# Kernel tuning notes

Hardware: AMD Instinct MI355X
Metric: run time of the kernel (lower is better)

Reference implementation:

```python
import jax, jax.numpy as jnp
import numpy as np

B, T, D_MODEL, N_HEADS = 4, 2048, 1024, 16
D_K = D_MODEL // N_HEADS


def setup_inputs() -> dict:
    key = jax.random.key(0)
    kx, kq, kk, kv, ko = jax.random.split(key, 5)
    scale = 1.0 / np.sqrt(D_MODEL)  # ~ torch Linear init scale
    return {
        "x": jax.random.normal(kx, (B, T, D_MODEL), dtype=jnp.float32),
        "W_q": jax.random.uniform(kq, (D_MODEL, D_MODEL), jnp.float32, -scale, scale),
        "W_k": jax.random.uniform(kk, (D_MODEL, D_MODEL), jnp.float32, -scale, scale),
        "W_v": jax.random.uniform(kv, (D_MODEL, D_MODEL), jnp.float32, -scale, scale),
        "W_o": jax.random.uniform(ko, (D_MODEL, D_MODEL), jnp.float32, -scale, scale),
    }


def reference(x, W_q, W_k, W_v, W_o):
    b, t, _ = x.shape
    # nn.Linear(y) = y @ W.T ; split to (B, H, T, d_k)
    def split_heads(y):
        return y.reshape(b, t, N_HEADS, D_K).transpose(0, 2, 1, 3)

    Q = split_heads(x @ W_q.T)
    K = split_heads(x @ W_k.T)
    V = split_heads(x @ W_v.T)

    scores = jnp.einsum("bhqd,bhkd->bhqk", Q, K) / jnp.sqrt(jnp.float32(D_K))
    causal = jnp.triu(jnp.ones((t, t), dtype=bool), k=1)  # True = masked
    scores = jnp.where(causal, -jnp.inf, scores)
    weights = jax.nn.softmax(scores, axis=-1)
    out = jnp.einsum("bhqk,bhkd->bhqd", weights, V)
    out = out.transpose(0, 2, 1, 3).reshape(b, t, D_MODEL)
    return out @ W_o.T
```

## Files before the change

### kernel.cpp

```cpp
#include <hip/hip_runtime.h>

typedef __attribute__((ext_vector_type(8))) short s16x8;
typedef __attribute__((ext_vector_type(4))) float fx4;
typedef __attribute__((ext_vector_type(4))) int ix4;

#define B_SZ 4
#define T_SZ 2048
#define DM 1024
#define NH 16
#define DK 64
#define M_SZ (B_SZ * T_SZ)
#define NINF (-__builtin_inff())
#define QSCALE (0.125f * 1.44269504088896340736f)

__device__ __forceinline__ unsigned short f2bf(float f) {
    unsigned int u = __float_as_uint(f);
    unsigned int r = u + 0x7fffu + ((u >> 16) & 1u);
    return (unsigned short)(r >> 16);
}

__device__ __forceinline__ unsigned cvtpk(float lo, float hi) {
    unsigned r;
    asm("v_cvt_pk_bf16_f32 %0, %1, %2" : "=v"(r) : "v"(lo), "v"(hi));
    return r;
}

__device__ __forceinline__ void async16(const unsigned short* g, unsigned short* l) {
    __builtin_amdgcn_global_load_lds(
        (const __attribute__((address_space(1))) unsigned int*)g,
        (__attribute__((address_space(3))) unsigned int*)l, 16, 0, 0);
}

__device__ __forceinline__ void barrier_nodrain() {
    asm volatile("" ::: "memory");
    __builtin_amdgcn_s_barrier();
    asm volatile("" ::: "memory");
}

__global__ void cast_all(const float* __restrict__ x,
                         const float* __restrict__ s1, const float* __restrict__ s2,
                         const float* __restrict__ s3, const float* __restrict__ s4,
                         unsigned short* __restrict__ xb, unsigned short* __restrict__ wb) {
    const int y = blockIdx.y;
    const float* s;
    unsigned short* d;
    int n;
    if (y == 0) { s = x; d = xb; n = M_SZ * DM; }
    else {
        s = (y == 1) ? s1 : (y == 2) ? s2 : (y == 3) ? s3 : s4;
        d = wb + (size_t)(y - 1) * (DM * DM);
        n = DM * DM;
    }
    int i = (blockIdx.x * blockDim.x + threadIdx.x) * 4;
    int stride = gridDim.x * blockDim.x * 4;
    for (; i + 3 < n; i += stride) {
        float4 v = *(const float4*)(s + i);
        ushort4 o;
        o.x = f2bf(v.x); o.y = f2bf(v.y); o.z = f2bf(v.z); o.w = f2bf(v.w);
        *(ushort4*)(d + i) = o;
    }
}

__global__ __launch_bounds__(512, 2) void gemm_qkv256(const unsigned short* __restrict__ A,
                                                      const unsigned short* __restrict__ W,
                                                      unsigned short* __restrict__ Qs,
                                                      unsigned short* __restrict__ Kb,
                                                      unsigned short* __restrict__ Vt) {
    __shared__ __align__(16) unsigned short S[49152];

    const int t = threadIdx.x;
    const int lane = t & 63, w = t >> 6;
    const int wm = w >> 2, wn = w & 3;
    const int lrow = lane & 15, lk = lane >> 4;
    const int bx = blockIdx.x;
    const int m0 = blockIdx.y * 128;
    const int K = DM;
    const int NKT = K / 64;

    fx4 acc[4][4] = {};

    const int srow = t >> 3;
    const int cs = (t & 7) ^ (srow & 7);
    const unsigned short* Ag = A + (long)(m0 + srow) * K + cs * 8;
    const unsigned short* Bg = W + (long)(bx * 256 + srow) * K + cs * 8;

    async16(Ag,           &S[t * 8]);
    async16(Ag + 64 * K,  &S[4096 + t * 8]);
    async16(Bg,           &S[16384 + t * 8]);
    async16(Bg + 64 * K,  &S[16384 + 4096 + t * 8]);
    async16(Bg + 128 * K, &S[16384 + 8192 + t * 8]);
    async16(Bg + 192 * K, &S[16384 + 12288 + t * 8]);

    for (int kt = 0; kt < NKT; ++kt) {
        const int cur = kt & 1;
        if (kt + 1 < NKT) {
            const int ko = (kt + 1) * 64;
            const int nbA = (cur ^ 1) * 8192;
            const int nbB = 16384 + (cur ^ 1) * 16384;
            async16(Ag + ko,           &S[nbA + t * 8]);
            async16(Ag + 64 * K + ko,  &S[nbA + 4096 + t * 8]);
            async16(Bg + ko,           &S[nbB + t * 8]);
            async16(Bg + 64 * K + ko,  &S[nbB + 4096 + t * 8]);
            async16(Bg + 128 * K + ko, &S[nbB + 8192 + t * 8]);
            async16(Bg + 192 * K + ko, &S[nbB + 12288 + t * 8]);
            asm volatile("s_waitcnt vmcnt(6)" ::: "memory");
        } else {
            asm volatile("s_waitcnt vmcnt(0)" ::: "memory");
        }
        barrier_nodrain();
        const unsigned short* Ab = &S[cur * 8192];
        const unsigned short* Bb = &S[16384 + cur * 16384];
#pragma unroll
        for (int kk = 0; kk < 2; ++kk) {
            const int sw = ((kk * 4 + lk) ^ (lrow & 7)) * 8;
            s16x8 af[4], bf[4];
#pragma unroll
            for (int mf = 0; mf < 4; ++mf)
                af[mf] = *(const s16x8*)&Ab[(wm * 64 + mf * 16 + lrow) * 64 + sw];
#pragma unroll
            for (int nf = 0; nf < 4; ++nf)
                bf[nf] = *(const s16x8*)&Bb[(wn * 64 + nf * 16 + lrow) * 64 + sw];
            __builtin_amdgcn_s_setprio(1);
#pragma unroll
            for (int mf = 0; mf < 4; ++mf)
#pragma unroll
                for (int nf = 0; nf < 4; ++nf)
                    acc[mf][nf] = __builtin_amdgcn_mfma_f32_16x16x32_bf16(af[mf], bf[nf], acc[mf][nf], 0, 0, 0);
            __builtin_amdgcn_s_setprio(0);
        }
        barrier_nodrain();
    }

    const int which = bx >> 2;
    const int n0l = (bx & 3) * 256;
    if (which < 2) {
        unsigned short* dst = which ? Kb : Qs;
        const float sc = which ? 1.f : QSCALE;
#pragma unroll
        for (int mf = 0; mf < 4; ++mf)
#pragma unroll
            for (int nf = 0; nf < 4; ++nf)
#pragma unroll
                for (int r = 0; r < 4; ++r) {
                    int row = m0 + wm * 64 + mf * 16 + lk * 4 + r;
                    int col = n0l + wn * 64 + nf * 16 + lrow;
                    dst[(long)row * DM + col] = f2bf(acc[mf][nf][r] * sc);
                }
    } else {
#pragma unroll
        for (int mf = 0; mf < 4; ++mf)
#pragma unroll
            for (int nf = 0; nf < 4; ++nf) {
                const int cl = wn * 64 + nf * 16 + lrow;
                const int rl = wm * 64 + mf * 16 + lk * 4;
                ushort4 pk;
                pk.x = f2bf(acc[mf][nf][0]); pk.y = f2bf(acc[mf][nf][1]);
                pk.z = f2bf(acc[mf][nf][2]); pk.w = f2bf(acc[mf][nf][3]);
                *(ushort4*)&S[cl * 132 + rl] = pk;
            }
        __syncthreads();
        const int c = t >> 1, h2 = t & 1;
        unsigned short* vtp = Vt + (long)(n0l + c) * M_SZ + m0 + h2 * 64;
#pragma unroll
        for (int j = 0; j < 8; ++j) {
            union { struct { ushort4 a, b; } s; ix4 v; } u;
            u.s.a = *(const ushort4*)&S[c * 132 + h2 * 64 + j * 8];
            u.s.b = *(const ushort4*)&S[c * 132 + h2 * 64 + j * 8 + 4];
            *(ix4*)(vtp + j * 8) = u.v;
        }
    }
}

__global__ __launch_bounds__(512, 2) void gemm_out256(const unsigned short* __restrict__ A,
                                                      const unsigned short* __restrict__ W,
                                                      float* __restrict__ C) {
    __shared__ __align__(16) unsigned short S[49152];

    const int t = threadIdx.x;
    const int lane = t & 63, w = t >> 6;
    const int wm = w >> 2, wn = w & 3;
    const int lrow = lane & 15, lk = lane >> 4;
    const int n0 = blockIdx.x * 256;
    const int m0 = blockIdx.y * 128;
    const int K = DM;
    const int NKT = K / 64;

    fx4 acc[4][4] = {};

    const int srow = t >> 3;
    const int cs = (t & 7) ^ (srow & 7);
    const unsigned short* Ag = A + (long)(m0 + srow) * K + cs * 8;
    const unsigned short* Bg = W + (long)(n0 + srow) * K + cs * 8;

    async16(Ag,           &S[t * 8]);
    async16(Ag + 64 * K,  &S[4096 + t * 8]);
    async16(Bg,           &S[16384 + t * 8]);
    async16(Bg + 64 * K,  &S[16384 + 4096 + t * 8]);
    async16(Bg + 128 * K, &S[16384 + 8192 + t * 8]);
    async16(Bg + 192 * K, &S[16384 + 12288 + t * 8]);

    for (int kt = 0; kt < NKT; ++kt) {
        const int cur = kt & 1;
        if (kt + 1 < NKT) {
            const int ko = (kt + 1) * 64;
            const int nbA = (cur ^ 1) * 8192;
            const int nbB = 16384 + (cur ^ 1) * 16384;
            async16(Ag + ko,           &S[nbA + t * 8]);
            async16(Ag + 64 * K + ko,  &S[nbA + 4096 + t * 8]);
            async16(Bg + ko,           &S[nbB + t * 8]);
            async16(Bg + 64 * K + ko,  &S[nbB + 4096 + t * 8]);
            async16(Bg + 128 * K + ko, &S[nbB + 8192 + t * 8]);
            async16(Bg + 192 * K + ko, &S[nbB + 12288 + t * 8]);
            asm volatile("s_waitcnt vmcnt(6)" ::: "memory");
        } else {
            asm volatile("s_waitcnt vmcnt(0)" ::: "memory");
        }
        barrier_nodrain();
        const unsigned short* Ab = &S[cur * 8192];
        const unsigned short* Bb = &S[16384 + cur * 16384];
#pragma unroll
        for (int kk = 0; kk < 2; ++kk) {
            const int sw = ((kk * 4 + lk) ^ (lrow & 7)) * 8;
            s16x8 af[4], bf[4];
#pragma unroll
            for (int mf = 0; mf < 4; ++mf)
                af[mf] = *(const s16x8*)&Ab[(wm * 64 + mf * 16 + lrow) * 64 + sw];
#pragma unroll
            for (int nf = 0; nf < 4; ++nf)
                bf[nf] = *(const s16x8*)&Bb[(wn * 64 + nf * 16 + lrow) * 64 + sw];
            __builtin_amdgcn_s_setprio(1);
#pragma unroll
            for (int mf = 0; mf < 4; ++mf)
#pragma unroll
                for (int nf = 0; nf < 4; ++nf)
                    acc[mf][nf] = __builtin_amdgcn_mfma_f32_16x16x32_bf16(af[mf], bf[nf], acc[mf][nf], 0, 0, 0);
            __builtin_amdgcn_s_setprio(0);
        }
        barrier_nodrain();
    }

#pragma unroll
    for (int mf = 0; mf < 4; ++mf)
#pragma unroll
        for (int nf = 0; nf < 4; ++nf)
#pragma unroll
            for (int r = 0; r < 4; ++r) {
                int row = m0 + wm * 64 + mf * 16 + lk * 4 + r;
                int col = n0 + wn * 64 + nf * 16 + lrow;
                C[(long)row * DM + col] = acc[mf][nf][r];
            }
}

__global__ __launch_bounds__(256, 4) void attn_kernel(const unsigned short* __restrict__ Q,
                                                      const unsigned short* __restrict__ Kb,
                                                      const unsigned short* __restrict__ Vt,
                                                      unsigned short* __restrict__ O) {
    __shared__ __align__(16) unsigned short Ks[2][64 * 64];
    __shared__ __align__(16) unsigned short Vs[2][64 * 64];
    __shared__ __align__(16) unsigned short Pl[4][16 * 64];

    const int t = threadIdx.x;
    const int lane = t & 63, w = t >> 6;
    const int lrow = lane & 15, lk = lane >> 4;
    const int hb = blockIdx.x;
    const int h = hb & 15, b = hb >> 4;
    const int qb = 15 - blockIdx.y;
    const int row0 = b * T_SZ;
    const int q0w = qb * 128 + w * 32;

    s16x8 qf[2][2];
#pragma unroll
    for (int hh = 0; hh < 2; ++hh) {
        const unsigned short* qp = Q + (long)(row0 + q0w + hh * 16 + lrow) * DM + h * DK + lk * 8;
        qf[hh][0] = *(const s16x8*)qp;
        qf[hh][1] = *(const s16x8*)(qp + 32);
    }

    fx4 acc[2][4] = {};
    float mrun[2] = {NINF, NINF}, lsum[2] = {0.f, 0.f};

    const int srow = t >> 3;
    const int chk = (t & 7) ^ (srow & 7);
    const unsigned short* Kg = Kb + (long)(row0 + srow) * DM + h * DK + chk * 8;
    const unsigned short* Vg = Vt + (long)(h * DK + srow) * M_SZ + row0 + chk * 8;
    unsigned short* Kl = &Ks[0][t * 8];
    unsigned short* Vl = &Vs[0][t * 8];

    const int nt = 2 * qb + 2;

    async16(Kg, Kl);
    async16(Kg + 32 * DM, Kl + 2048);
    async16(Vg, Vl);
    async16(Vg + 32 * (long)M_SZ, Vl + 2048);
    asm volatile("s_waitcnt vmcnt(0)" ::: "memory");
    __syncthreads();

    for (int kt = 0; kt < nt; ++kt) {
        const int cur = kt & 1;
        const bool pre = (kt + 1 < nt);
        if (pre) {
            const long koff = (long)(kt + 1) * 64 * DM;
            const int voff = (kt + 1) * 64;
            async16(Kg + koff, Kl + (cur ^ 1) * 4096);
            async16(Kg + koff + 32 * DM, Kl + (cur ^ 1) * 4096 + 2048);
            async16(Vg + voff, Vl + (cur ^ 1) * 4096);
            async16(Vg + voff + 32 * (long)M_SZ, Vl + (cur ^ 1) * 4096 + 2048);
        }
        const int kv0 = kt * 64;
        if (kv0 <= q0w + 31) {
            const char* ksb = (const char*)&Ks[cur][0];
            float p[2][4][4];
#pragma unroll
            for (int sub = 0; sub < 4; ++sub) {
                const int kv0s = kv0 + sub * 16;
                if (kv0s <= q0w + 31) {
                    const int rb = (sub * 16 + lrow) << 7;
                    const int sw = (lrow & 7) << 4;
                    const s16x8 kf0 = *(const s16x8*)(ksb + (rb + ((lk * 16) ^ sw)));
                    const s16x8 kf1 = *(const s16x8*)(ksb + (rb + ((64 + lk * 16) ^ sw)));
                    fx4 s1 = {};
                    s1 = __builtin_amdgcn_mfma_f32_16x16x32_bf16(kf0, qf[1][0], s1, 0, 0, 0);
                    s1 = __builtin_amdgcn_mfma_f32_16x16x32_bf16(kf1, qf[1][1], s1, 0, 0, 0);
                    if (kv0s + 15 > q0w + 16) {
#pragma unroll
                        for (int r = 0; r < 4; ++r)
                            if (kv0s + lk * 4 + r > q0w + 16 + lrow) s1[r] = NINF;
                    }
#pragma unroll
                    for (int r = 0; r < 4; ++r) p[1][sub][r] = s1[r];
                    if (kv0s <= q0w + 15) {
                        fx4 s0 = {};
                        s0 = __builtin_amdgcn_mfma_f32_16x16x32_bf16(kf0, qf[0][0], s0, 0, 0, 0);
                        s0 = __builtin_amdgcn_mfma_f32_16x16x32_bf16(kf1, qf[0][1], s0, 0, 0, 0);
                        if (kv0s + 15 > q0w) {
#pragma unroll
                            for (int r = 0; r < 4; ++r)
                                if (kv0s + lk * 4 + r > q0w + lrow) s0[r] = NINF;
                        }
#pragma unroll
                        for (int r = 0; r < 4; ++r) p[0][sub][r] = s0[r];
                    } else {
#pragma unroll
                        for (int r = 0; r < 4; ++r) p[0][sub][r] = NINF;
                    }
                } else {
#pragma unroll
                    for (int r = 0; r < 4; ++r) { p[0][sub][r] = NINF; p[1][sub][r] = NINF; }
                }
            }
#pragma unroll
            for (int hh = 0; hh < 2; ++hh) {
                float m0 = fmaxf(fmaxf(p[hh][0][0], p[hh][0][1]), fmaxf(p[hh][0][2], p[hh][0][3]));
                float m1 = fmaxf(fmaxf(p[hh][1][0], p[hh][1][1]), fmaxf(p[hh][1][2], p[hh][1][3]));
                float m2 = fmaxf(fmaxf(p[hh][2][0], p[hh][2][1]), fmaxf(p[hh][2][2], p[hh][2][3]));
                float m3 = fmaxf(fmaxf(p[hh][3][0], p[hh][3][1]), fmaxf(p[hh][3][2], p[hh][3][3]));
                float pm = fmaxf(fmaxf(m0, m1), fmaxf(m2, m3));
                if (__any(pm > mrun[hh] + 8.f)) {
                    pm = fmaxf(pm, __shfl_xor(pm, 16));
                    pm = fmaxf(pm, __shfl_xor(pm, 32));
                    const float mnew = fmaxf(mrun[hh], pm);
                    const float sc = exp2f(mrun[hh] - mnew);
                    mrun[hh] = mnew;
                    lsum[hh] *= sc;
#pragma unroll
                    for (int r = 0; r < 4; ++r) {
                        const float scr = __shfl(sc, lk * 4 + r);
                        acc[hh][0][r] *= scr; acc[hh][1][r] *= scr;
                        acc[hh][2][r] *= scr; acc[hh][3][r] *= scr;
                    }
                }
#pragma unroll
                for (int sub = 0; sub < 4; ++sub)
#pragma unroll
                    for (int r = 0; r < 4; ++r)
                        p[hh][sub][r] = exp2f(p[hh][sub][r] - mrun[hh]);
                float a0 = (p[hh][0][0] + p[hh][0][1]) + (p[hh][0][2] + p[hh][0][3]);
                float a1 = (p[hh][1][0] + p[hh][1][1]) + (p[hh][1][2] + p[hh][1][3]);
                float a2 = (p[hh][2][0] + p[hh][2][1]) + (p[hh][2][2] + p[hh][2][3]);
                float a3 = (p[hh][3][0] + p[hh][3][1]) + (p[hh][3][2] + p[hh][3][3]);
                lsum[hh] += (a0 + a1) + (a2 + a3);
            }
            s16x8 pf[2][2];
#pragma unroll
            for (int hh = 0; hh < 2; ++hh) {
#pragma unroll
                for (int sub = 0; sub < 4; ++sub) {
                    uint2 pw;
                    pw.x = cvtpk(p[hh][sub][0], p[hh][sub][1]);
                    pw.y = cvtpk(p[hh][sub][2], p[hh][sub][3]);
                    *(uint2*)&Pl[w][lrow * 64 + ((sub * 16 + lk * 4) ^ ((lrow & 7) << 3))] = pw;
                }
                pf[hh][0] = *(const s16x8*)&Pl[w][lrow * 64 + ((lk * 8) ^ ((lrow & 7) << 3))];
                pf[hh][1] = *(const s16x8*)&Pl[w][lrow * 64 + ((32 + lk * 8) ^ ((lrow & 7) << 3))];
            }
#pragma unroll
            for (int s = 0; s < 2; ++s) {
                if (kv0 + s * 32 <= q0w + 31) {
                    const bool h0a = (kv0 + s * 32 <= q0w + 15);
#pragma unroll
                    for (int nf = 0; nf < 4; ++nf) {
                        const int d = nf * 16 + lrow;
                        const s16x8 vf = *(const s16x8*)&Vs[cur][d * 64 + (((s * 4 + lk) ^ (lrow & 7)) << 3)];
                        if (h0a)
                            acc[0][nf] = __builtin_amdgcn_mfma_f32_16x16x32_bf16(pf[0][s], vf, acc[0][nf], 0, 0, 0);
                        acc[1][nf] = __builtin_amdgcn_mfma_f32_16x16x32_bf16(pf[1][s], vf, acc[1][nf], 0, 0, 0);
                    }
                }
            }
        }
        asm volatile("s_waitcnt vmcnt(0)" ::: "memory");
        __syncthreads();
    }

#pragma unroll
    for (int hh = 0; hh < 2; ++hh) {
        lsum[hh] += __shfl_xor(lsum[hh], 16);
        lsum[hh] += __shfl_xor(lsum[hh], 32);
        float linv[4];
#pragma unroll
        for (int r = 0; r < 4; ++r) linv[r] = 1.f / __shfl(lsum[hh], lk * 4 + r);
        unsigned short* op = O + (long)(row0 + q0w + hh * 16) * DM + h * DK;
#pragma unroll
        for (int nf = 0; nf < 4; ++nf)
#pragma unroll
            for (int r = 0; r < 4; ++r)
                op[(long)(lk * 4 + r) * DM + nf * 16 + lrow] = f2bf(acc[hh][nf][r] * linv[r]);
    }
}

extern "C" void kernel_launch(void* const* d_in, const int* in_sizes, int n_in,
                              void* d_out, int out_size, void* d_ws, size_t ws_size,
                              hipStream_t stream) {
    const float* x  = (const float*)d_in[0];
    const float* Wq = (const float*)d_in[1];
    const float* Wk = (const float*)d_in[2];
    const float* Wv = (const float*)d_in[3];
    const float* Wo = (const float*)d_in[4];
    float* out = (float*)d_out;

    unsigned short* wsu = (unsigned short*)d_ws;
    unsigned short* xb  = wsu;
    unsigned short* wqb = xb + 8388608;
    unsigned short* wob = wqb + 3 * 1048576;
    unsigned short* Qs  = wob + 1048576;
    unsigned short* Ob  = Qs + 8388608;

    unsigned short* Kb = (unsigned short*)d_out;
    unsigned short* Vt = Kb + 8388608;

    cast_all<<<dim3(512, 5), 256, 0, stream>>>(x, Wq, Wk, Wv, Wo, xb, wqb);

    gemm_qkv256<<<dim3(12, M_SZ / 128), 512, 0, stream>>>(xb, wqb, Qs, Kb, Vt);

    dim3 agrid(64, 16);
    attn_kernel<<<agrid, 256, 0, stream>>>(Qs, Kb, Vt, Ob);

    gemm_out256<<<dim3(DM / 256, M_SZ / 128), 512, 0, stream>>>(Ob, wob, out);
}
```

Baseline: 178.6 us.

## Triple-buffer GEMM loads and compute softmax row sums with MFMA

Both projection GEMMs move from double to triple buffering in shared memory, prefetching two K-tiles ahead with adjusted vmcnt waits, to hide more global load latency. Shared memory per block grows from 96KB to 144KB, which may prevent two blocks fitting per CU. In attention, the softmax denominator is now accumulated by an MFMA of the bf16 probabilities against a ones vector, replacing per-lane float adds and the final cross-lane shuffles. The max reduction is also regrouped into three-input max operations. The MFMA row sum uses bf16-rounded probabilities, matching the values used in the PV product.

```diff
diff --git a/kernel.cpp b/kernel.cpp
--- a/kernel.cpp
+++ b/kernel.cpp
@@ -12,6 +12,7 @@
 #define M_SZ (B_SZ * T_SZ)
 #define NINF (-__builtin_inff())
 #define QSCALE (0.125f * 1.44269504088896340736f)
+#define MAX3(a,b,c) fmaxf(fmaxf(a,b),c)
 
 __device__ __forceinline__ unsigned short f2bf(float f) {
     unsigned int u = __float_as_uint(f);
@@ -66,7 +67,7 @@
                                                       unsigned short* __restrict__ Qs,
                                                       unsigned short* __restrict__ Kb,
                                                       unsigned short* __restrict__ Vt) {
-    __shared__ __align__(16) unsigned short S[49152];
+    __shared__ __align__(16) unsigned short S[73728];
 
     const int t = threadIdx.x;
     const int lane = t & 63, w = t >> 6;
@@ -84,32 +85,41 @@
     const unsigned short* Ag = A + (long)(m0 + srow) * K + cs * 8;
     const unsigned short* Bg = W + (long)(bx * 256 + srow) * K + cs * 8;
 
-    async16(Ag,           &S[t * 8]);
-    async16(Ag + 64 * K,  &S[4096 + t * 8]);
-    async16(Bg,           &S[16384 + t * 8]);
-    async16(Bg + 64 * K,  &S[16384 + 4096 + t * 8]);
-    async16(Bg + 128 * K, &S[16384 + 8192 + t * 8]);
-    async16(Bg + 192 * K, &S[16384 + 12288 + t * 8]);
-
+#pragma unroll
+    for (int pt = 0; pt < 2; ++pt) {
+        const int ko = pt * 64;
+        const int nbA = pt * 8192;
+        const int nbB = 24576 + pt * 16384;
+        async16(Ag + ko,           &S[nbA + t * 8]);
+        async16(Ag + 64 * K + ko,  &S[nbA + 4096 + t * 8]);
+        async16(Bg + ko,           &S[nbB + t * 8]);
+        async16(Bg + 64 * K + ko,  &S[nbB + 4096 + t * 8]);
+        async16(Bg + 128 * K + ko, &S[nbB + 8192 + t * 8]);
+        async16(Bg + 192 * K + ko, &S[nbB + 12288 + t * 8]);
+    }
+
+    int cur = 0;
     for (int kt = 0; kt < NKT; ++kt) {
-        const int cur = kt & 1;
-        if (kt + 1 < NKT) {
-            const int ko = (kt + 1) * 64;
-            const int nbA = (cur ^ 1) * 8192;
-            const int nbB = 16384 + (cur ^ 1) * 16384;
+        if (kt + 2 < NKT) {
+            int stg = cur + 2; if (stg >= 3) stg -= 3;
+            const int ko = (kt + 2) * 64;
+            const int nbA = stg * 8192;
+            const int nbB = 24576 + stg * 16384;
             async16(Ag + ko,           &S[nbA + t * 8]);
             async16(Ag + 64 * K + ko,  &S[nbA + 4096 + t * 8]);
             async16(Bg + ko,           &S[nbB + t * 8]);
             async16(Bg + 64 * K + ko,  &S[nbB + 4096 + t * 8]);
             async16(Bg + 128 * K + ko, &S[nbB + 8192 + t * 8]);
             async16(Bg + 192 * K + ko, &S[nbB + 12288 + t * 8]);
+            asm volatile("s_waitcnt vmcnt(12)" ::: "memory");
+        } else if (kt + 1 < NKT) {
             asm volatile("s_waitcnt vmcnt(6)" ::: "memory");
         } else {
             asm volatile("s_waitcnt vmcnt(0)" ::: "memory");
         }
         barrier_nodrain();
         const unsigned short* Ab = &S[cur * 8192];
-        const unsigned short* Bb = &S[16384 + cur * 16384];
+        const unsigned short* Bb = &S[24576 + cur * 16384];
 #pragma unroll
         for (int kk = 0; kk < 2; ++kk) {
             const int sw = ((kk * 4 + lk) ^ (lrow & 7)) * 8;
@@ -129,6 +139,7 @@
             __builtin_amdgcn_s_setprio(0);
         }
         barrier_nodrain();
+        cur = (cur + 1 == 3) ? 0 : cur + 1;
     }
 
     const int which = bx >> 2;
@@ -174,7 +185,7 @@
 __global__ __launch_bounds__(512, 2) void gemm_out256(const unsigned short* __restrict__ A,
                                                       const unsigned short* __restrict__ W,
                                                       float* __restrict__ C) {
-    __shared__ __align__(16) unsigned short S[49152];
+    __shared__ __align__(16) unsigned short S[73728];
 
     const int t = threadIdx.x;
     const int lane = t & 63, w = t >> 6;
@@ -192,32 +203,41 @@
     const unsigned short* Ag = A + (long)(m0 + srow) * K + cs * 8;
     const unsigned short* Bg = W + (long)(n0 + srow) * K + cs * 8;
 
-    async16(Ag,           &S[t * 8]);
-    async16(Ag + 64 * K,  &S[4096 + t * 8]);
-    async16(Bg,           &S[16384 + t * 8]);
-    async16(Bg + 64 * K,  &S[16384 + 4096 + t * 8]);
-    async16(Bg + 128 * K, &S[16384 + 8192 + t * 8]);
-    async16(Bg + 192 * K, &S[16384 + 12288 + t * 8]);
-
+#pragma unroll
+    for (int pt = 0; pt < 2; ++pt) {
+        const int ko = pt * 64;
+        const int nbA = pt * 8192;
+        const int nbB = 24576 + pt * 16384;
+        async16(Ag + ko,           &S[nbA + t * 8]);
+        async16(Ag + 64 * K + ko,  &S[nbA + 4096 + t * 8]);
+        async16(Bg + ko,           &S[nbB + t * 8]);
+        async16(Bg + 64 * K + ko,  &S[nbB + 4096 + t * 8]);
+        async16(Bg + 128 * K + ko, &S[nbB + 8192 + t * 8]);
+        async16(Bg + 192 * K + ko, &S[nbB + 12288 + t * 8]);
+    }
+
+    int cur = 0;
     for (int kt = 0; kt < NKT; ++kt) {
-        const int cur = kt & 1;
-        if (kt + 1 < NKT) {
-            const int ko = (kt + 1) * 64;
-            const int nbA = (cur ^ 1) * 8192;
-            const int nbB = 16384 + (cur ^ 1) * 16384;
+        if (kt + 2 < NKT) {
+            int stg = cur + 2; if (stg >= 3) stg -= 3;
+            const int ko = (kt + 2) * 64;
+            const int nbA = stg * 8192;
+            const int nbB = 24576 + stg * 16384;
             async16(Ag + ko,           &S[nbA + t * 8]);
             async16(Ag + 64 * K + ko,  &S[nbA + 4096 + t * 8]);
             async16(Bg + ko,           &S[nbB + t * 8]);
             async16(Bg + 64 * K + ko,  &S[nbB + 4096 + t * 8]);
             async16(Bg + 128 * K + ko, &S[nbB + 8192 + t * 8]);
             async16(Bg + 192 * K + ko, &S[nbB + 12288 + t * 8]);
+            asm volatile("s_waitcnt vmcnt(12)" ::: "memory");
+        } else if (kt + 1 < NKT) {
             asm volatile("s_waitcnt vmcnt(6)" ::: "memory");
         } else {
             asm volatile("s_waitcnt vmcnt(0)" ::: "memory");
         }
         barrier_nodrain();
         const unsigned short* Ab = &S[cur * 8192];
-        const unsigned short* Bb = &S[16384 + cur * 16384];
+        const unsigned short* Bb = &S[24576 + cur * 16384];
 #pragma unroll
         for (int kk = 0; kk < 2; ++kk) {
             const int sw = ((kk * 4 + lk) ^ (lrow & 7)) * 8;
@@ -237,6 +257,7 @@
             __builtin_amdgcn_s_setprio(0);
         }
         barrier_nodrain();
+        cur = (cur + 1 == 3) ? 0 : cur + 1;
     }
 
 #pragma unroll
@@ -276,8 +297,12 @@
         qf[hh][1] = *(const s16x8*)(qp + 32);
     }
 
+    const short onebf = (short)0x3F80;
+    const s16x8 ones = {onebf, onebf, onebf, onebf, onebf, onebf, onebf, onebf};
+
     fx4 acc[2][4] = {};
-    float mrun[2] = {NINF, NINF}, lsum[2] = {0.f, 0.f};
+    fx4 suml[2] = {};
+    float mrun[2] = {NINF, NINF};
 
     const int srow = t >> 3;
     const int chk = (t & 7) ^ (srow & 7);
@@ -350,23 +375,24 @@
             }
 #pragma unroll
             for (int hh = 0; hh < 2; ++hh) {
-                float m0 = fmaxf(fmaxf(p[hh][0][0], p[hh][0][1]), fmaxf(p[hh][0][2], p[hh][0][3]));
-                float m1 = fmaxf(fmaxf(p[hh][1][0], p[hh][1][1]), fmaxf(p[hh][1][2], p[hh][1][3]));
-                float m2 = fmaxf(fmaxf(p[hh][2][0], p[hh][2][1]), fmaxf(p[hh][2][2], p[hh][2][3]));
-                float m3 = fmaxf(fmaxf(p[hh][3][0], p[hh][3][1]), fmaxf(p[hh][3][2], p[hh][3][3]));
-                float pm = fmaxf(fmaxf(m0, m1), fmaxf(m2, m3));
+                float t0 = MAX3(p[hh][0][0], p[hh][0][1], p[hh][0][2]);
+                float t1 = MAX3(p[hh][0][3], p[hh][1][0], p[hh][1][1]);
+                float t2 = MAX3(p[hh][1][2], p[hh][1][3], p[hh][2][0]);
+                float t3 = MAX3(p[hh][2][1], p[hh][2][2], p[hh][2][3]);
+                float t4 = MAX3(p[hh][3][0], p[hh][3][1], p[hh][3][2]);
+                float pm = fmaxf(MAX3(MAX3(t0, t1, t2), t3, t4), p[hh][3][3]);
                 if (__any(pm > mrun[hh] + 8.f)) {
                     pm = fmaxf(pm, __shfl_xor(pm, 16));
                     pm = fmaxf(pm, __shfl_xor(pm, 32));
                     const float mnew = fmaxf(mrun[hh], pm);
                     const float sc = exp2f(mrun[hh] - mnew);
                     mrun[hh] = mnew;
-                    lsum[hh] *= sc;
 #pragma unroll
                     for (int r = 0; r < 4; ++r) {
                         const float scr = __shfl(sc, lk * 4 + r);
                         acc[hh][0][r] *= scr; acc[hh][1][r] *= scr;
                         acc[hh][2][r] *= scr; acc[hh][3][r] *= scr;
+                        suml[hh][r] *= scr;
                     }
                 }
 #pragma unroll
@@ -374,11 +400,6 @@
 #pragma unroll
                     for (int r = 0; r < 4; ++r)
                         p[hh][sub][r] = exp2f(p[hh][sub][r] - mrun[hh]);
-                float a0 = (p[hh][0][0] + p[hh][0][1]) + (p[hh][0][2] + p[hh][0][3]);
-                float a1 = (p[hh][1][0] + p[hh][1][1]) + (p[hh][1][2] + p[hh][1][3]);
-                float a2 = (p[hh][2][0] + p[hh][2][1]) + (p[hh][2][2] + p[hh][2][3]);
-                float a3 = (p[hh][3][0] + p[hh][3][1]) + (p[hh][3][2] + p[hh][3][3]);
-                lsum[hh] += (a0 + a1) + (a2 + a3);
             }
             s16x8 pf[2][2];
 #pragma unroll
@@ -397,6 +418,9 @@
             for (int s = 0; s < 2; ++s) {
                 if (kv0 + s * 32 <= q0w + 31) {
                     const bool h0a = (kv0 + s * 32 <= q0w + 15);
+                    if (h0a)
+                        suml[0] = __builtin_amdgcn_mfma_f32_16x16x32_bf16(pf[0][s], ones, suml[0], 0, 0, 0);
+                    suml[1] = __builtin_amdgcn_mfma_f32_16x16x32_bf16(pf[1][s], ones, suml[1], 0, 0, 0);
 #pragma unroll
                     for (int nf = 0; nf < 4; ++nf) {
                         const int d = nf * 16 + lrow;
@@ -414,11 +438,9 @@
 
 #pragma unroll
     for (int hh = 0; hh < 2; ++hh) {
-        lsum[hh] += __shfl_xor(lsum[hh], 16);
-        lsum[hh] += __shfl_xor(lsum[hh], 32);
         float linv[4];
 #pragma unroll
-        for (int r = 0; r < 4; ++r) linv[r] = 1.f / __shfl(lsum[hh], lk * 4 + r);
+        for (int r = 0; r < 4; ++r) linv[r] = 1.f / suml[hh][r];
         unsigned short* op = O + (long)(row0 + q0w + hh * 16) * DM + h * DK;
 #pragma unroll
         for (int nf = 0; nf < 4; ++nf)
```

New measurement: 180.5 us. About the same (+1.0%).
